# Optimization experiments

Hardware: AMD Instinct MI355X
Metric: run time of the kernel (lower is better)

## Reference

```python
import jax, jax.numpy as jnp
import numpy as np
from jax import lax


def setup_inputs() -> dict:
    key = jax.random.key(0)
    k1, k2 = jax.random.split(key)
    B, C, H, W = 4, 32, 512, 512
    x = jax.random.normal(k1, (B, C, H, W), dtype=jnp.float32)
    # offset conv params: out_ch = 2*k*k = 18 (init: small weights, zero bias)
    w_off = jax.random.normal(k2, (18, C, 3, 3), dtype=jnp.float32) * 0.05
    b_off = jnp.zeros((18,), dtype=jnp.float32)
    return {"x": x, "w_off": w_off, "b_off": b_off}


def _grid_sample_bilinear_zeros(x, grid):
    # x: (B,C,H,W); grid: (B,H,W,2) in [-1,1], align_corners=True, zeros padding
    B, C, H, W = x.shape
    ix = (grid[..., 0] + 1.0) * 0.5 * (W - 1)  # (B,H,W)
    iy = (grid[..., 1] + 1.0) * 0.5 * (H - 1)
    x0 = jnp.floor(ix); y0 = jnp.floor(iy)
    x1 = x0 + 1.0;      y1 = y0 + 1.0
    wx1 = ix - x0; wx0 = 1.0 - wx1
    wy1 = iy - y0; wy0 = 1.0 - wy1
    bi = jnp.arange(B)[:, None, None]

    def corner(yc, xc, w):
        valid = (xc >= 0) & (xc <= W - 1) & (yc >= 0) & (yc <= H - 1)
        xi = jnp.clip(xc, 0, W - 1).astype(jnp.int32)
        yi = jnp.clip(yc, 0, H - 1).astype(jnp.int32)
        v = x[bi, :, yi, xi]  # (B,H,W,C)
        return v * (w * valid.astype(x.dtype))[..., None]

    out = (corner(y0, x0, wy0 * wx0) + corner(y0, x1, wy0 * wx1)
           + corner(y1, x0, wy1 * wx0) + corner(y1, x1, wy1 * wx1))
    return out.transpose(0, 3, 1, 2)  # (B,C,H,W)


def reference(x, w_off, b_off):
    B, C, H, W = x.shape
    # offset conv: 3x3, stride 1, padding 1 (shape-preserving)
    off = lax.conv_general_dilated(
        x, w_off, window_strides=(1, 1), padding=((1, 1), (1, 1)),
        dimension_numbers=("NCHW", "OIHW", "NCHW"))
    off = off + b_off[None, :, None, None]               # (B,18,H,W)
    off = off.transpose(0, 2, 3, 1).reshape(B, H, W, 9, 2)
    # base integer grid: (x, y) per pixel
    gy, gx = jnp.meshgrid(jnp.arange(H, dtype=x.dtype),
                          jnp.arange(W, dtype=x.dtype), indexing="ij")
    base = jnp.stack([gx, gy], axis=-1)                  # (H,W,2)
    g = base[None, :, :, None, :] + off                  # (B,H,W,9,2)
    g = g / jnp.array([W - 1, H - 1], dtype=x.dtype) * 2.0 - 1.0
    g = g[:, :, :, 0, :]                                 # only first kernel offset used
    return _grid_sample_bilinear_zeros(x, g)
```

## Files before the change

kernel.cpp:

```cpp
#include <hip/hip_runtime.h>

#define BB 4
#define CC 32
#define HH 512
#define WW 512
#define PLANE ((size_t)HH * WW)
#define NPIX ((size_t)BB * HH * WW)

__global__ __launch_bounds__(256) void conv_off_kernel(
    const float* __restrict__ x, const float* __restrict__ w_off,
    const float* __restrict__ b_off, float* __restrict__ off) {
  const int nb = gridDim.x;
  const int i  = blockIdx.x;
  const int j  = (i & 7) * (nb >> 3) + (i >> 3);
  const int b    = j >> 8;
  const int row0 = (j & 255) << 1;

  const int t    = threadIdx.x;
  const int w4   = (t & 127) << 2;
  const int h    = row0 + (t >> 7);
  const int lane = t & 63;

  float4 a0v, a1v;
  a0v.x = a0v.y = a0v.z = a0v.w = b_off[0];
  a1v.x = a1v.y = a1v.z = a1v.w = b_off[1];

  const float* xb = x + (size_t)b * CC * PLANE + (size_t)h * WW + w4;

  float4 mA[3], mB[3];
  float  eA[3], eB[3];

  auto load_ch = [&](int ci, float4* m, float* e) {
#pragma unroll
    for (int r = 0; r < 3; ++r) {
      const int hy = h - 1 + r;
      const float* q = xb + (size_t)ci * PLANE + (ptrdiff_t)(r - 1) * WW;
      if (hy >= 0 && hy < HH) {
        m[r] = *(const float4*)q;
        const float* ea = (lane == 0) ? q - 1 : q + 4;
        const bool eok = (lane == 0) ? (w4 > 0)
                                     : (lane == 63 && w4 < WW - 4);
        e[r] = eok ? *ea : 0.f;
      } else {
        m[r].x = m[r].y = m[r].z = m[r].w = 0.f;
        e[r] = 0.f;
      }
    }
  };

  auto compute_ch = [&](int ci, const float4* m, const float* e) {
    const float* wp0 = w_off + ci * 9;
    const float* wp1 = w_off + 288 + ci * 9;
#pragma unroll
    for (int kh = 0; kh < 3; ++kh) {
      float vl = __shfl_up(m[kh].w, 1);
      if (lane == 0) vl = e[kh];
      float vr = __shfl_down(m[kh].x, 1);
      if (lane == 63) vr = e[kh];
      const float a0 = wp0[kh * 3 + 0], a1 = wp0[kh * 3 + 1], a2 = wp0[kh * 3 + 2];
      const float c0 = wp1[kh * 3 + 0], c1 = wp1[kh * 3 + 1], c2 = wp1[kh * 3 + 2];
      a0v.x += vl * a0 + m[kh].x * a1 + m[kh].y * a2;
      a0v.y += m[kh].x * a0 + m[kh].y * a1 + m[kh].z * a2;
      a0v.z += m[kh].y * a0 + m[kh].z * a1 + m[kh].w * a2;
      a0v.w += m[kh].z * a0 + m[kh].w * a1 + vr * a2;
      a1v.x += vl * c0 + m[kh].x * c1 + m[kh].y * c2;
      a1v.y += m[kh].x * c0 + m[kh].y * c1 + m[kh].z * c2;
      a1v.z += m[kh].y * c0 + m[kh].z * c1 + m[kh].w * c2;
      a1v.w += m[kh].z * c0 + m[kh].w * c1 + vr * c2;
    }
  };

  load_ch(0, mA, eA);
  for (int ci = 0; ci < CC - 2; ci += 2) {
    load_ch(ci + 1, mB, eB);
    compute_ch(ci, mA, eA);
    load_ch(ci + 2, mA, eA);
    compute_ch(ci + 1, mB, eB);
  }
  load_ch(CC - 1, mB, eB);
  compute_ch(CC - 2, mA, eA);
  compute_ch(CC - 1, mB, eB);

  const size_t idx = ((size_t)b * HH + h) * WW + w4;
  *(float4*)(off + idx) = a0v;
  *(float4*)(off + NPIX + idx) = a1v;
}

__global__ __launch_bounds__(256) void sample_kernel(
    const float* __restrict__ x, const float* __restrict__ off,
    float* __restrict__ out) {
  const int nb = gridDim.x;
  const int i  = blockIdx.x;
  const int j  = (i & 7) * (nb >> 3) + (i >> 3);
  const size_t tid = (size_t)j * 256 + threadIdx.x;

  const int w = (int)(tid & (WW - 1));
  const int h = (int)((tid >> 9) & (HH - 1));
  const int b = (int)(tid >> 18);

  const float ix = (float)w + off[tid];
  const float iy = (float)h + off[NPIX + tid];

  const float x0f = floorf(ix);
  const float y0f = floorf(iy);

  const float wx1 = ix - x0f;
  const float wx0 = 1.f - wx1;
  const float wy1 = iy - y0f;
  const float wy0 = 1.f - wy1;

  const bool vx0 = (x0f >= 0.f) && (x0f <= (float)(WW - 1));
  const bool vx1 = (x0f + 1.f >= 0.f) && (x0f + 1.f <= (float)(WW - 1));
  const bool vy0 = (y0f >= 0.f) && (y0f <= (float)(HH - 1));
  const bool vy1 = (y0f + 1.f >= 0.f) && (y0f + 1.f <= (float)(HH - 1));

  const int xi0 = (int)fminf(fmaxf(x0f, 0.f), (float)(WW - 1));
  const int xi1 = (int)fminf(fmaxf(x0f + 1.f, 0.f), (float)(WW - 1));
  const int yi0 = (int)fminf(fmaxf(y0f, 0.f), (float)(HH - 1));
  const int yi1 = (int)fminf(fmaxf(y0f + 1.f, 0.f), (float)(HH - 1));

  const float w00 = wy0 * wx0 * ((vy0 && vx0) ? 1.f : 0.f);
  const float w01 = wy0 * wx1 * ((vy0 && vx1) ? 1.f : 0.f);
  const float w10 = wy1 * wx0 * ((vy1 && vx0) ? 1.f : 0.f);
  const float w11 = wy1 * wx1 * ((vy1 && vx1) ? 1.f : 0.f);

  const int i00 = yi0 * WW + xi0;
  const int i01 = yi0 * WW + xi1;
  const int i10 = yi1 * WW + xi0;
  const int i11 = yi1 * WW + xi1;

  const float* xp = x + (size_t)b * CC * PLANE;
  float* ob = out + (size_t)b * CC * PLANE + (size_t)h * WW + w;

#pragma unroll
  for (int half = 0; half < 2; ++half) {
    float v00[16], v01[16], v10[16], v11[16];
    const float* p = xp;
#pragma unroll
    for (int c = 0; c < 16; ++c) {
      v00[c] = p[i00];
      v01[c] = p[i01];
      v10[c] = p[i10];
      v11[c] = p[i11];
      p += PLANE;
    }
    float* o = ob;
#pragma unroll
    for (int c = 0; c < 16; ++c) {
      const float v = w00 * v00[c] + w01 * v01[c] + w10 * v10[c] + w11 * v11[c];
      __builtin_nontemporal_store(v, o);
      o += PLANE;
    }
    xp += (size_t)16 * PLANE;
    ob += (size_t)16 * PLANE;
  }
}

extern "C" void kernel_launch(void* const* d_in, const int* in_sizes, int n_in,
                              void* d_out, int out_size, void* d_ws, size_t ws_size,
                              hipStream_t stream) {
  const float* x     = (const float*)d_in[0];
  const float* w_off = (const float*)d_in[1];
  const float* b_off = (const float*)d_in[2];
  float* out = (float*)d_out;
  float* off = (float*)d_ws;

  conv_off_kernel<<<1024, 256, 0, stream>>>(x, w_off, b_off, off);

  const int nblk = (int)(NPIX / 256);
  sample_kernel<<<nblk, 256, 0, stream>>>(x, off, out);
}
```

Baseline: 303.6 us.

## Fuse offset conv and bilinear sampling into one kernel with paired loads

Merges the offset convolution and the grid-sample kernels, so each thread computes offsets for 4 pixels in registers and samples them directly. This removes the workspace round trip for the offset maps and one kernel launch. Corner fetches become 8-byte paired loads of adjacent x columns, with the weights redistributed so the edges stay correct, and outputs are written as float4 nontemporal stores. The trade-off is fewer threads (1024 blocks) each doing 4 pixels of gathers, which may reduce memory-level parallelism for the random-access sampling phase.

```diff
diff --git a/kernel.cpp b/kernel.cpp
--- a/kernel.cpp
+++ b/kernel.cpp
@@ -5,11 +5,12 @@
 #define HH 512
 #define WW 512
 #define PLANE ((size_t)HH * WW)
-#define NPIX ((size_t)BB * HH * WW)
 
-__global__ __launch_bounds__(256) void conv_off_kernel(
+typedef float fx4 __attribute__((ext_vector_type(4)));
+
+__global__ __launch_bounds__(256) void deform_fused_kernel(
     const float* __restrict__ x, const float* __restrict__ w_off,
-    const float* __restrict__ b_off, float* __restrict__ off) {
+    const float* __restrict__ b_off, float* __restrict__ out) {
   const int nb = gridDim.x;
   const int i  = blockIdx.x;
   const int j  = (i & 7) * (nb >> 3) + (i >> 3);
@@ -81,78 +82,70 @@
   compute_ch(CC - 2, mA, eA);
   compute_ch(CC - 1, mB, eB);
 
-  const size_t idx = ((size_t)b * HH + h) * WW + w4;
-  *(float4*)(off + idx) = a0v;
-  *(float4*)(off + NPIX + idx) = a1v;
-}
-
-__global__ __launch_bounds__(256) void sample_kernel(
-    const float* __restrict__ x, const float* __restrict__ off,
-    float* __restrict__ out) {
-  const int nb = gridDim.x;
-  const int i  = blockIdx.x;
-  const int j  = (i & 7) * (nb >> 3) + (i >> 3);
-  const size_t tid = (size_t)j * 256 + threadIdx.x;
-
-  const int w = (int)(tid & (WW - 1));
-  const int h = (int)((tid >> 9) & (HH - 1));
-  const int b = (int)(tid >> 18);
-
-  const float ix = (float)w + off[tid];
-  const float iy = (float)h + off[NPIX + tid];
-
-  const float x0f = floorf(ix);
-  const float y0f = floorf(iy);
-
-  const float wx1 = ix - x0f;
-  const float wx0 = 1.f - wx1;
-  const float wy1 = iy - y0f;
-  const float wy0 = 1.f - wy1;
-
-  const bool vx0 = (x0f >= 0.f) && (x0f <= (float)(WW - 1));
-  const bool vx1 = (x0f + 1.f >= 0.f) && (x0f + 1.f <= (float)(WW - 1));
-  const bool vy0 = (y0f >= 0.f) && (y0f <= (float)(HH - 1));
-  const bool vy1 = (y0f + 1.f >= 0.f) && (y0f + 1.f <= (float)(HH - 1));
-
-  const int xi0 = (int)fminf(fmaxf(x0f, 0.f), (float)(WW - 1));
-  const int xi1 = (int)fminf(fmaxf(x0f + 1.f, 0.f), (float)(WW - 1));
-  const int yi0 = (int)fminf(fmaxf(y0f, 0.f), (float)(HH - 1));
-  const int yi1 = (int)fminf(fmaxf(y0f + 1.f, 0.f), (float)(HH - 1));
-
-  const float w00 = wy0 * wx0 * ((vy0 && vx0) ? 1.f : 0.f);
-  const float w01 = wy0 * wx1 * ((vy0 && vx1) ? 1.f : 0.f);
-  const float w10 = wy1 * wx0 * ((vy1 && vx0) ? 1.f : 0.f);
-  const float w11 = wy1 * wx1 * ((vy1 && vx1) ? 1.f : 0.f);
-
-  const int i00 = yi0 * WW + xi0;
-  const int i01 = yi0 * WW + xi1;
-  const int i10 = yi1 * WW + xi0;
-  const int i11 = yi1 * WW + xi1;
+  float A0[4], A1[4], B0[4], B1[4];
+  int   r0[4], r1[4];
+  const float offx[4] = {a0v.x, a0v.y, a0v.z, a0v.w};
+  const float offy[4] = {a1v.x, a1v.y, a1v.z, a1v.w};
+#pragma unroll
+  for (int p = 0; p < 4; ++p) {
+    const float ix = (float)(w4 + p) + offx[p];
+    const float iy = (float)h + offy[p];
+    const float x0f = floorf(ix);
+    const float y0f = floorf(iy);
+    const float wx1 = ix - x0f, wx0 = 1.f - wx1;
+    const float wy1 = iy - y0f, wy0 = 1.f - wy1;
+    const bool vx0 = (x0f >= 0.f) && (x0f <= (float)(WW - 1));
+    const bool vx1 = (x0f + 1.f >= 0.f) && (x0f + 1.f <= (float)(WW - 1));
+    const bool vy0 = (y0f >= 0.f) && (y0f <= (float)(HH - 1));
+    const bool vy1 = (y0f + 1.f >= 0.f) && (y0f + 1.f <= (float)(HH - 1));
+    const int xi0 = (int)fminf(fmaxf(x0f, 0.f), (float)(WW - 1));
+    const int xi1 = (int)fminf(fmaxf(x0f + 1.f, 0.f), (float)(WW - 1));
+    const int yi0 = (int)fminf(fmaxf(y0f, 0.f), (float)(HH - 1));
+    const int yi1 = (int)fminf(fmaxf(y0f + 1.f, 0.f), (float)(HH - 1));
+    const float w00 = wy0 * wx0 * ((vy0 && vx0) ? 1.f : 0.f);
+    const float w01 = wy0 * wx1 * ((vy0 && vx1) ? 1.f : 0.f);
+    const float w10 = wy1 * wx0 * ((vy1 && vx0) ? 1.f : 0.f);
+    const float w11 = wy1 * wx1 * ((vy1 && vx1) ? 1.f : 0.f);
+    const int xL = (int)fminf(fmaxf(x0f, 0.f), (float)(WW - 2));
+    const int s0 = (xi0 > xL) ? 1 : 0;
+    const int s1 = (xi1 > xL) ? 1 : 0;
+    A0[p] = (s0 ? 0.f : w00) + (s1 ? 0.f : w01);
+    A1[p] = (s0 ? w00 : 0.f) + (s1 ? w01 : 0.f);
+    B0[p] = (s0 ? 0.f : w10) + (s1 ? 0.f : w11);
+    B1[p] = (s0 ? w10 : 0.f) + (s1 ? w11 : 0.f);
+    r0[p] = yi0 * WW + xL;
+    r1[p] = yi1 * WW + xL;
+  }
 
   const float* xp = x + (size_t)b * CC * PLANE;
-  float* ob = out + (size_t)b * CC * PLANE + (size_t)h * WW + w;
+  float* ob = out + (size_t)b * CC * PLANE + (size_t)h * WW + w4;
 
+#pragma unroll 1
+  for (int cg = 0; cg < 8; ++cg) {
+    float2 t0[4][4], t1[4][4];
+    const float* pc = xp;
 #pragma unroll
-  for (int half = 0; half < 2; ++half) {
-    float v00[16], v01[16], v10[16], v11[16];
-    const float* p = xp;
+    for (int c = 0; c < 4; ++c) {
 #pragma unroll
-    for (int c = 0; c < 16; ++c) {
-      v00[c] = p[i00];
-      v01[c] = p[i01];
-      v10[c] = p[i10];
-      v11[c] = p[i11];
-      p += PLANE;
+      for (int p = 0; p < 4; ++p) {
+        __builtin_memcpy(&t0[c][p], pc + r0[p], 8);
+        __builtin_memcpy(&t1[c][p], pc + r1[p], 8);
+      }
+      pc += PLANE;
     }
     float* o = ob;
 #pragma unroll
-    for (int c = 0; c < 16; ++c) {
-      const float v = w00 * v00[c] + w01 * v01[c] + w10 * v10[c] + w11 * v11[c];
-      __builtin_nontemporal_store(v, o);
+    for (int c = 0; c < 4; ++c) {
+      fx4 v;
+      v.x = t0[c][0].x * A0[0] + t0[c][0].y * A1[0] + t1[c][0].x * B0[0] + t1[c][0].y * B1[0];
+      v.y = t0[c][1].x * A0[1] + t0[c][1].y * A1[1] + t1[c][1].x * B0[1] + t1[c][1].y * B1[1];
+      v.z = t0[c][2].x * A0[2] + t0[c][2].y * A1[2] + t1[c][2].x * B0[2] + t1[c][2].y * B1[2];
+      v.w = t0[c][3].x * A0[3] + t0[c][3].y * A1[3] + t1[c][3].x * B0[3] + t1[c][3].y * B1[3];
+      __builtin_nontemporal_store(v, (fx4*)o);
       o += PLANE;
     }
-    xp += (size_t)16 * PLANE;
-    ob += (size_t)16 * PLANE;
+    xp += (size_t)4 * PLANE;
+    ob += (size_t)4 * PLANE;
   }
 }
 
@@ -163,10 +156,6 @@
   const float* w_off = (const float*)d_in[1];
   const float* b_off = (const float*)d_in[2];
   float* out = (float*)d_out;
-  float* off = (float*)d_ws;
 
-  conv_off_kernel<<<1024, 256, 0, stream>>>(x, w_off, b_off, off);
-
-  const int nblk = (int)(NPIX / 256);
-  sample_kernel<<<nblk, 256, 0, stream>>>(x, off, out);
+  deform_fused_kernel<<<1024, 256, 0, stream>>>(x, w_off, b_off, out);
 }
```

Result: no change. 298.4 us (-1.7%).
